# Performance work log

Measured on AMD Instinct MI355X. Metric: run time of the kernel, lower is better.

## Reference

```python
import jax, jax.numpy as jnp
import numpy as np
from functools import partial

B, IN, H, OUT, DEPTH = 4096, 1024, 2048, 1024, 8


def setup_inputs() -> dict:
    key = jax.random.key(0)
    ks = jax.random.split(key, 20)
    r = lambda k, shape: jax.random.normal(k, shape, dtype=jnp.float32)
    return {
        "x":  r(ks[0], (B, IN)),
        "W0": r(ks[1], (IN, H)) / np.sqrt(IN),  "b0": r(ks[2], (H,)) * 0.01,
        "W1": r(ks[3], (H, H)) / np.sqrt(H),    "b1": r(ks[4], (H,)) * 0.01,
        "cw1": r(ks[5], (DEPTH, H, H)), "cb1": r(ks[6], (H,)),
        "KW1": r(ks[7], (H, H)) / np.sqrt(H),  "Kb1": r(ks[8], (H,)) * 0.01,
        "W2": r(ks[9], (H, H)) / np.sqrt(H),   "b2": r(ks[10], (H,)) * 0.01,
        "cw2": r(ks[11], (DEPTH, H, H)), "cb2": r(ks[12], (H,)),
        "KW2": r(ks[13], (H, H)) / np.sqrt(H), "Kb2": r(ks[14], (H,)) * 0.01,
        "W3": r(ks[15], (H, OUT)) / np.sqrt(H), "b3": r(ks[16], (OUT,)) * 0.01,
    }


def _cosmic_processing(cw, batch, n_in, n_out):
    # state starts uniform over the n_in-dim 'cosmic' register, one per output j
    s0 = jnp.full((n_out, n_in), 1.0 / np.sqrt(n_in), dtype=cw.dtype)
    angles = cw[:, :, :3]  # (depth, n_out, 3): consciousness/intelligence/wisdom angles

    def step(s, ang):  # s: (n_out, n_in), ang: (n_out, 3)
        # circulant rotation: (M s)[i] = cos*s[i] - sin*s[i+1] + sin*s[i-1]
        for k in range(3):
            c = jnp.cos(ang[:, k])[:, None]
            si = jnp.sin(ang[:, k])[:, None]
            s = c * s - si * jnp.roll(s, -1, axis=1) + si * jnp.roll(s, 1, axis=1)
        return s, None

    s, _ = jax.lax.scan(step, s0, angles)
    prob = jnp.abs(s[:, 0]) ** 2  # (n_out,), sample-independent
    return jnp.broadcast_to(prob[None, :], (batch, n_out))


def _cosmic_layer(x, cw, cb, KW, Kb):
    classical = x @ KW + Kb
    cosmic = _cosmic_processing(cw, x.shape[0], x.shape[1], KW.shape[1])
    return jnp.tanh(classical + cosmic)


def reference(x, W0, b0, W1, b1, cw1, cb1, KW1, Kb1,
              W2, b2, cw2, cb2, KW2, Kb2, W3, b3):
    h = jax.nn.relu(x @ W0 + b0)
    h = jax.nn.relu(h @ W1 + b1)
    h = _cosmic_layer(h, cw1, cb1, KW1, Kb1)
    h = jax.nn.relu(h @ W2 + b2)
    h = _cosmic_layer(h, cw2, cb2, KW2, Kb2)
    return jax.nn.relu(h @ W3 + b3)
```

## Files before the change

### kernel.cpp

```cpp
#include <hip/hip_runtime.h>
#include <math.h>


typedef _Float16 f16;
typedef _Float16 f16x8 __attribute__((ext_vector_type(8)));
typedef _Float16 f16x4 __attribute__((ext_vector_type(4)));
typedef float f32x4 __attribute__((ext_vector_type(4)));

#define GLD16(gp, lp) __builtin_amdgcn_global_load_lds( \
    (const __attribute__((address_space(1))) unsigned int*)(gp), \
    (__attribute__((address_space(3))) unsigned int*)(lp), 16, 0, 0)

__global__ void cast_f32_f16(const float* __restrict__ in, f16* __restrict__ out, int n4) {
  int i = blockIdx.x * 256 + threadIdx.x;
  if (i < n4) {
    float4 v = ((const float4*)in)[i];
    f16x4 o = { (f16)v.x, (f16)v.y, (f16)v.z, (f16)v.w };
    ((f16x4*)out)[i] = o;
  }
}

struct TD { const float* src; f16* dst; int K; int N; };
struct TD6 { TD d[6]; };

__global__ void cast_transpose6(TD6 a) {
  TD d = a.d[blockIdx.z];
  int bx = blockIdx.x * 32, by = blockIdx.y * 32;
  if (bx >= d.N || by >= d.K) return;
  __shared__ float tile[32][33];
  int tx = threadIdx.x & 31, ty = threadIdx.x >> 5;
#pragma unroll
  for (int r = ty; r < 32; r += 8)
    tile[r][tx] = d.src[(size_t)(by + r) * d.N + bx + tx];
  __syncthreads();
#pragma unroll
  for (int r = ty; r < 32; r += 8)
    d.dst[(size_t)(bx + r) * d.K + by + tx] = (f16)tile[tx][r];
}

__global__ void cosmic_prob(const float* __restrict__ cw, float* __restrict__ prob, int H) {
  int r = blockIdx.x * 256 + threadIdx.x;
  if (r >= H) return;
  float p = 1.0f;
#pragma unroll
  for (int d = 0; d < 8; ++d) {
    const float* a = cw + ((size_t)d * H + r) * H;
    p *= cosf(a[0]) * cosf(a[1]) * cosf(a[2]);
  }
  prob[r] = p * p / (float)H;
}

template <int EPI>
__global__ __launch_bounds__(512, 2)
void gemm_f16(const f16* __restrict__ A, const f16* __restrict__ BT,
              const float* __restrict__ bias, const float* __restrict__ prob,
              f16* __restrict__ Ch, float* __restrict__ Cf,
              int M, int N, int K, int GX) {
  __shared__ f16 lds[3 * 16384 + 3 * 8192];
  f16* As = lds;
  f16* Bs = lds + 3 * 16384;

  const int t = threadIdx.x;

  const int nwg = gridDim.x;
  const int bid = blockIdx.x;
  const int swz = (bid & 7) * (nwg >> 3) + (bid >> 3);
  const int bx = swz % GX;
  const int by = swz / GX;
  const int m0 = by * 256;
  const int n0 = bx * 128;

  auto stage = [&](int kt, int buf) {
    const int k0 = kt << 6;
#pragma unroll
    for (int q = 0; q < 4; ++q) {
      int Fh = q * 4096 + t * 8;
      int r = Fh >> 6;
      int c = (Fh >> 3) & 7;
      const f16* src = A + (size_t)(m0 + r) * K + k0 + ((c ^ (r & 7)) << 3);
      GLD16(src, As + buf * 16384 + Fh);
    }
#pragma unroll
    for (int q = 0; q < 2; ++q) {
      int Fh = q * 4096 + t * 8;
      int r = Fh >> 6;
      int c = (Fh >> 3) & 7;
      const f16* src = BT + (size_t)(n0 + r) * K + k0 + ((c ^ (r & 7)) << 3);
      GLD16(src, Bs + buf * 8192 + Fh);
    }
  };

  const int wave = t >> 6, lane = t & 63;
  const int wr = wave >> 1, wc = wave & 1;
  const int kg = lane >> 4, rc = lane & 15;

  f32x4 acc[4][4] = {};

  auto compute = [&](int buf) {
    const f16* Ab = As + buf * 16384;
    const f16* Bb = Bs + buf * 8192;
    f16x8 af[2][4], bf[2][4];
#pragma unroll
    for (int s = 0; s < 2; ++s) {
      const int cc = s * 4 + kg;
#pragma unroll
      for (int i = 0; i < 4; ++i) {
        int row = wr * 64 + i * 16 + rc;
        af[s][i] = *(const f16x8*)&Ab[row * 64 + ((cc ^ (row & 7)) << 3)];
      }
#pragma unroll
      for (int n = 0; n < 4; ++n) {
        int row = wc * 64 + n * 16 + rc;
        bf[s][n] = *(const f16x8*)&Bb[row * 64 + ((cc ^ (row & 7)) << 3)];
      }
    }
    __builtin_amdgcn_s_setprio(1);
#pragma unroll
    for (int s = 0; s < 2; ++s)
#pragma unroll
      for (int i = 0; i < 4; ++i)
#pragma unroll
        for (int n = 0; n < 4; ++n)
          acc[i][n] = __builtin_amdgcn_mfma_f32_16x16x32_f16(af[s][i], bf[s][n], acc[i][n], 0, 0, 0);
    __builtin_amdgcn_s_setprio(0);
  };

  const int nt = K >> 6;
  stage(0, 0);
  stage(1, 1);
  int cur = 0;
  for (int kt = 0; kt < nt - 1; ++kt) {
    asm volatile("s_waitcnt vmcnt(6) lgkmcnt(0)" ::: "memory");
    __builtin_amdgcn_s_barrier();
    if (kt + 2 < nt) {
      int sb = cur + 2; if (sb >= 3) sb -= 3;
      stage(kt + 2, sb);
    }
    compute(cur);
    cur = (cur + 1 == 3) ? 0 : cur + 1;
  }
  asm volatile("s_waitcnt vmcnt(0) lgkmcnt(0)" ::: "memory");
  __builtin_amdgcn_s_barrier();
  compute(cur);

#pragma unroll
  for (int n = 0; n < 4; ++n) {
    const int col = n0 + wc * 64 + n * 16 + rc;
    float bn = bias[col];
    if (EPI == 1) bn += prob[col];
#pragma unroll
    for (int i = 0; i < 4; ++i) {
      const int row = m0 + wr * 64 + i * 16 + kg * 4;
#pragma unroll
      for (int q = 0; q < 4; ++q) {
        float v = acc[i][n][q] + bn;
        if (EPI == 1) v = tanhf(v);
        else v = fmaxf(v, 0.0f);
        if (EPI == 2) Cf[(size_t)(row + q) * N + col] = v;
        else Ch[(size_t)(row + q) * N + col] = (f16)v;
      }
    }
  }
}

extern "C" void kernel_launch(void* const* d_in, const int* in_sizes, int n_in,
                              void* d_out, int out_size, void* d_ws, size_t ws_size,
                              hipStream_t stream) {
  const float* x   = (const float*)d_in[0];
  const float* W0  = (const float*)d_in[1];
  const float* b0  = (const float*)d_in[2];
  const float* W1  = (const float*)d_in[3];
  const float* b1  = (const float*)d_in[4];
  const float* cw1 = (const float*)d_in[5];
  const float* KW1 = (const float*)d_in[7];
  const float* Kb1 = (const float*)d_in[8];
  const float* W2  = (const float*)d_in[9];
  const float* b2  = (const float*)d_in[10];
  const float* cw2 = (const float*)d_in[11];
  const float* KW2 = (const float*)d_in[13];
  const float* Kb2 = (const float*)d_in[14];
  const float* W3  = (const float*)d_in[15];
  const float* b3  = (const float*)d_in[16];

  const int B = 4096, IN = 1024, H = 2048, OUT = 1024;

  char* ws = (char*)d_ws;
  size_t off = 0;
  auto alloc = [&](size_t bytes) {
    char* p = ws + off;
    off = (off + bytes + 255) & ~(size_t)255;
    return p;
  };
  f16* xh    = (f16*)alloc((size_t)B * IN * 2);
  f16* W0T   = (f16*)alloc((size_t)H * IN * 2);
  f16* W1T   = (f16*)alloc((size_t)H * H * 2);
  f16* KW1T  = (f16*)alloc((size_t)H * H * 2);
  f16* W2T   = (f16*)alloc((size_t)H * H * 2);
  f16* KW2T  = (f16*)alloc((size_t)H * H * 2);
  f16* W3T   = (f16*)alloc((size_t)OUT * H * 2);
  f16* hA    = (f16*)alloc((size_t)B * H * 2);
  f16* hB    = (f16*)alloc((size_t)B * H * 2);
  float* p1  = (float*)alloc((size_t)H * 4);
  float* p2  = (float*)alloc((size_t)H * 4);
  (void)ws_size;

  cast_f32_f16<<<(B * IN / 4 + 255) / 256, 256, 0, stream>>>(x, xh, B * IN / 4);

  TD6 td;
  td.d[0] = { W0,  W0T,  IN, H };
  td.d[1] = { W1,  W1T,  H,  H };
  td.d[2] = { KW1, KW1T, H,  H };
  td.d[3] = { W2,  W2T,  H,  H };
  td.d[4] = { KW2, KW2T, H,  H };
  td.d[5] = { W3,  W3T,  H,  OUT };
  cast_transpose6<<<dim3(H / 32, H / 32, 6), 256, 0, stream>>>(td);

  cosmic_prob<<<(H + 255) / 256, 256, 0, stream>>>(cw1, p1, H);
  cosmic_prob<<<(H + 255) / 256, 256, 0, stream>>>(cw2, p2, H);

  auto launch = [&](int epi, const f16* Aq, const f16* BTq, const float* bi,
                    const float* pr, f16* Co, float* Cfo, int N_, int K_) {
    int gx = N_ / 128, gy = B / 256;
    dim3 grid(gx * gy);
    if (epi == 0) gemm_f16<0><<<grid, 512, 0, stream>>>(Aq, BTq, bi, pr, Co, Cfo, B, N_, K_, gx);
    else if (epi == 1) gemm_f16<1><<<grid, 512, 0, stream>>>(Aq, BTq, bi, pr, Co, Cfo, B, N_, K_, gx);
    else gemm_f16<2><<<grid, 512, 0, stream>>>(Aq, BTq, bi, pr, Co, Cfo, B, N_, K_, gx);
  };

  launch(0, xh, W0T, b0,  nullptr, hA, nullptr, H,   IN);
  launch(0, hA, W1T, b1,  nullptr, hB, nullptr, H,   H);
  launch(1, hB, KW1T, Kb1, p1,     hA, nullptr, H,   H);
  launch(0, hA, W2T, b2,  nullptr, hB, nullptr, H,   H);
  launch(1, hB, KW2T, Kb2, p2,     hA, nullptr, H,   H);
  launch(2, hA, W3T, b3,  nullptr, nullptr, (float*)d_out, OUT, H);
}
```

Baseline: 249.9 us.

## Switch GEMM to 32x32x16 MFMA with interleaved staging and smaller final tile

```diff
diff --git a/kernel.cpp b/kernel.cpp
--- a/kernel.cpp
+++ b/kernel.cpp
@@ -5,7 +5,7 @@
 typedef _Float16 f16;
 typedef _Float16 f16x8 __attribute__((ext_vector_type(8)));
 typedef _Float16 f16x4 __attribute__((ext_vector_type(4)));
-typedef float f32x4 __attribute__((ext_vector_type(4)));
+typedef float f32x16 __attribute__((ext_vector_type(16)));
 
 #define GLD16(gp, lp) __builtin_amdgcn_global_load_lds( \
     (const __attribute__((address_space(1))) unsigned int*)(gp), \
@@ -38,27 +38,34 @@
     d.dst[(size_t)(bx + r) * d.K + by + tx] = (f16)tile[tx][r];
 }
 
-__global__ void cosmic_prob(const float* __restrict__ cw, float* __restrict__ prob, int H) {
+__global__ void cosmic_pp(const float* __restrict__ cw, float* __restrict__ pp, int H) {
+  int i = blockIdx.x * 256 + threadIdx.x;
+  if (i >= 8 * H) return;
+  const float* a = cw + (size_t)i * H;
+  pp[i] = cosf(a[0]) * cosf(a[1]) * cosf(a[2]);
+}
+__global__ void cosmic_fin(const float* __restrict__ pp, float* __restrict__ prob, int H) {
   int r = blockIdx.x * 256 + threadIdx.x;
   if (r >= H) return;
   float p = 1.0f;
 #pragma unroll
-  for (int d = 0; d < 8; ++d) {
-    const float* a = cw + ((size_t)d * H + r) * H;
-    p *= cosf(a[0]) * cosf(a[1]) * cosf(a[2]);
-  }
+  for (int d = 0; d < 8; ++d) p *= pp[d * H + r];
   prob[r] = p * p / (float)H;
 }
 
-template <int EPI>
+template <int EPI, int BM>
 __global__ __launch_bounds__(512, 2)
 void gemm_f16(const f16* __restrict__ A, const f16* __restrict__ BT,
               const float* __restrict__ bias, const float* __restrict__ prob,
               f16* __restrict__ Ch, float* __restrict__ Cf,
               int M, int N, int K, int GX) {
-  __shared__ f16 lds[3 * 16384 + 3 * 8192];
+  constexpr int ASZ = BM * 64;
+  constexpr int BSZ = 128 * 64;
+  constexpr int MB  = BM / 128;
+  constexpr int RA  = BM / 64;
+  __shared__ f16 lds[3 * (ASZ + BSZ)];
   f16* As = lds;
-  f16* Bs = lds + 3 * 16384;
+  f16* Bs = lds + 3 * ASZ;
 
   const int t = threadIdx.x;
 
@@ -67,97 +74,105 @@
   const int swz = (bid & 7) * (nwg >> 3) + (bid >> 3);
   const int bx = swz % GX;
   const int by = swz / GX;
-  const int m0 = by * 256;
+  const int m0 = by * BM;
   const int n0 = bx * 128;
 
-  auto stage = [&](int kt, int buf) {
-    const int k0 = kt << 6;
-#pragma unroll
-    for (int q = 0; q < 4; ++q) {
-      int Fh = q * 4096 + t * 8;
-      int r = Fh >> 6;
-      int c = (Fh >> 3) & 7;
-      const f16* src = A + (size_t)(m0 + r) * K + k0 + ((c ^ (r & 7)) << 3);
-      GLD16(src, As + buf * 16384 + Fh);
-    }
-#pragma unroll
-    for (int q = 0; q < 2; ++q) {
-      int Fh = q * 4096 + t * 8;
-      int r = Fh >> 6;
-      int c = (Fh >> 3) & 7;
-      const f16* src = BT + (size_t)(n0 + r) * K + k0 + ((c ^ (r & 7)) << 3);
-      GLD16(src, Bs + buf * 8192 + Fh);
-    }
+  auto stageA = [&](int kt, int buf, int q) {
+    int F = q * 4096 + t * 8;
+    int r = F >> 6, c = (F >> 3) & 7;
+    const f16* src = A + (size_t)(m0 + r) * K + (kt << 6) + ((c ^ (r & 7)) << 3);
+    GLD16(src, As + buf * ASZ + F);
+  };
+  auto stageB = [&](int kt, int buf, int q) {
+    int F = q * 4096 + t * 8;
+    int r = F >> 6, c = (F >> 3) & 7;
+    const f16* src = BT + (size_t)(n0 + r) * K + (kt << 6) + ((c ^ (r & 7)) << 3);
+    GLD16(src, Bs + buf * BSZ + F);
+  };
+  auto stage_all = [&](int kt, int buf) {
+#pragma unroll
+    for (int q = 0; q < RA; ++q) stageA(kt, buf, q);
+#pragma unroll
+    for (int q = 0; q < 2; ++q) stageB(kt, buf, q);
   };
 
   const int wave = t >> 6, lane = t & 63;
   const int wr = wave >> 1, wc = wave & 1;
-  const int kg = lane >> 4, rc = lane & 15;
-
-  f32x4 acc[4][4] = {};
-
-  auto compute = [&](int buf) {
-    const f16* Ab = As + buf * 16384;
-    const f16* Bb = Bs + buf * 8192;
-    f16x8 af[2][4], bf[2][4];
-#pragma unroll
-    for (int s = 0; s < 2; ++s) {
-      const int cc = s * 4 + kg;
-#pragma unroll
-      for (int i = 0; i < 4; ++i) {
-        int row = wr * 64 + i * 16 + rc;
-        af[s][i] = *(const f16x8*)&Ab[row * 64 + ((cc ^ (row & 7)) << 3)];
+  const int rc = lane & 31, hi = lane >> 5;
+
+  f32x16 acc[MB][2] = {};
+
+  auto kphase = [&](int cur, int p, int stage_kt, int sb) {
+    const f16* Ab = As + cur * ASZ;
+    const f16* Bb = Bs + cur * BSZ;
+    const int cc = p * 2 + hi;
+    f16x8 a[MB], b[2];
+#pragma unroll
+    for (int mb = 0; mb < MB; ++mb) {
+      int row = wr * (BM / 4) + mb * 32 + rc;
+      a[mb] = *(const f16x8*)&Ab[row * 64 + ((cc ^ (row & 7)) << 3)];
+    }
+#pragma unroll
+    for (int nb = 0; nb < 2; ++nb) {
+      int row = wc * 64 + nb * 32 + rc;
+      b[nb] = *(const f16x8*)&Bb[row * 64 + ((cc ^ (row & 7)) << 3)];
+    }
+    if (stage_kt >= 0) {
+      if (BM == 256) {
+        stageA(stage_kt, sb, p);
+        if (p < 2) stageB(stage_kt, sb, p);
+      } else {
+        if (p < 2) stageA(stage_kt, sb, p);
+        else stageB(stage_kt, sb, p - 2);
       }
-#pragma unroll
-      for (int n = 0; n < 4; ++n) {
-        int row = wc * 64 + n * 16 + rc;
-        bf[s][n] = *(const f16x8*)&Bb[row * 64 + ((cc ^ (row & 7)) << 3)];
-      }
-    }
+    }
+    asm volatile("s_waitcnt lgkmcnt(0)" ::: "memory");
+    __builtin_amdgcn_sched_barrier(0);
     __builtin_amdgcn_s_setprio(1);
 #pragma unroll
-    for (int s = 0; s < 2; ++s)
-#pragma unroll
-      for (int i = 0; i < 4; ++i)
-#pragma unroll
-        for (int n = 0; n < 4; ++n)
-          acc[i][n] = __builtin_amdgcn_mfma_f32_16x16x32_f16(af[s][i], bf[s][n], acc[i][n], 0, 0, 0);
+    for (int mb = 0; mb < MB; ++mb)
+#pragma unroll
+      for (int nb = 0; nb < 2; ++nb)
+        acc[mb][nb] = __builtin_amdgcn_mfma_f32_32x32x16_f16(a[mb], b[nb], acc[mb][nb], 0, 0, 0);
     __builtin_amdgcn_s_setprio(0);
+    __builtin_amdgcn_sched_barrier(0);
   };
 
   const int nt = K >> 6;
-  stage(0, 0);
-  stage(1, 1);
+  stage_all(0, 0);
+  stage_all(1, 1);
   int cur = 0;
-  for (int kt = 0; kt < nt - 1; ++kt) {
-    asm volatile("s_waitcnt vmcnt(6) lgkmcnt(0)" ::: "memory");
+  for (int kt = 0; kt < nt; ++kt) {
+    if (kt + 1 < nt) {
+      if (BM == 256) asm volatile("s_waitcnt vmcnt(6)" ::: "memory");
+      else           asm volatile("s_waitcnt vmcnt(4)" ::: "memory");
+    } else {
+      asm volatile("s_waitcnt vmcnt(0)" ::: "memory");
+    }
     __builtin_amdgcn_s_barrier();
-    if (kt + 2 < nt) {
-      int sb = cur + 2; if (sb >= 3) sb -= 3;
-      stage(kt + 2, sb);
-    }
-    compute(cur);
+    int sb = cur + 2; if (sb >= 3) sb -= 3;
+    const int skt = (kt + 2 < nt) ? (kt + 2) : -1;
+#pragma unroll
+    for (int p = 0; p < 4; ++p) kphase(cur, p, skt, sb);
     cur = (cur + 1 == 3) ? 0 : cur + 1;
   }
-  asm volatile("s_waitcnt vmcnt(0) lgkmcnt(0)" ::: "memory");
-  __builtin_amdgcn_s_barrier();
-  compute(cur);
-
-#pragma unroll
-  for (int n = 0; n < 4; ++n) {
-    const int col = n0 + wc * 64 + n * 16 + rc;
+
+#pragma unroll
+  for (int nb = 0; nb < 2; ++nb) {
+    const int col = n0 + wc * 64 + nb * 32 + rc;
     float bn = bias[col];
     if (EPI == 1) bn += prob[col];
 #pragma unroll
-    for (int i = 0; i < 4; ++i) {
-      const int row = m0 + wr * 64 + i * 16 + kg * 4;
-#pragma unroll
-      for (int q = 0; q < 4; ++q) {
-        float v = acc[i][n][q] + bn;
+    for (int mb = 0; mb < MB; ++mb) {
+      const int rbase = m0 + wr * (BM / 4) + mb * 32 + 4 * hi;
+#pragma unroll
+      for (int r = 0; r < 16; ++r) {
+        const int row = rbase + (r & 3) + 8 * (r >> 2);
+        float v = acc[mb][nb][r] + bn;
         if (EPI == 1) v = tanhf(v);
         else v = fmaxf(v, 0.0f);
-        if (EPI == 2) Cf[(size_t)(row + q) * N + col] = v;
-        else Ch[(size_t)(row + q) * N + col] = (f16)v;
+        if (EPI == 2) Cf[(size_t)row * N + col] = v;
+        else Ch[(size_t)row * N + col] = (f16)v;
       }
     }
   }
@@ -202,6 +217,7 @@
   f16* hB    = (f16*)alloc((size_t)B * H * 2);
   float* p1  = (float*)alloc((size_t)H * 4);
   float* p2  = (float*)alloc((size_t)H * 4);
+  float* pp  = (float*)alloc((size_t)8 * H * 4);
   (void)ws_size;
 
   cast_f32_f16<<<(B * IN / 4 + 255) / 256, 256, 0, stream>>>(x, xh, B * IN / 4);
@@ -215,22 +231,23 @@
   td.d[5] = { W3,  W3T,  H,  OUT };
   cast_transpose6<<<dim3(H / 32, H / 32, 6), 256, 0, stream>>>(td);
 
-  cosmic_prob<<<(H + 255) / 256, 256, 0, stream>>>(cw1, p1, H);
-  cosmic_prob<<<(H + 255) / 256, 256, 0, stream>>>(cw2, p2, H);
-
-  auto launch = [&](int epi, const f16* Aq, const f16* BTq, const float* bi,
-                    const float* pr, f16* Co, float* Cfo, int N_, int K_) {
-    int gx = N_ / 128, gy = B / 256;
-    dim3 grid(gx * gy);
-    if (epi == 0) gemm_f16<0><<<grid, 512, 0, stream>>>(Aq, BTq, bi, pr, Co, Cfo, B, N_, K_, gx);
-    else if (epi == 1) gemm_f16<1><<<grid, 512, 0, stream>>>(Aq, BTq, bi, pr, Co, Cfo, B, N_, K_, gx);
-    else gemm_f16<2><<<grid, 512, 0, stream>>>(Aq, BTq, bi, pr, Co, Cfo, B, N_, K_, gx);
-  };
-
-  launch(0, xh, W0T, b0,  nullptr, hA, nullptr, H,   IN);
-  launch(0, hA, W1T, b1,  nullptr, hB, nullptr, H,   H);
-  launch(1, hB, KW1T, Kb1, p1,     hA, nullptr, H,   H);
-  launch(0, hA, W2T, b2,  nullptr, hB, nullptr, H,   H);
-  launch(1, hB, KW2T, Kb2, p2,     hA, nullptr, H,   H);
-  launch(2, hA, W3T, b3,  nullptr, nullptr, (float*)d_out, OUT, H);
-}
+  cosmic_pp<<<(8 * H + 255) / 256, 256, 0, stream>>>(cw1, pp, H);
+  cosmic_fin<<<(H + 255) / 256, 256, 0, stream>>>(pp, p1, H);
+  cosmic_pp<<<(8 * H + 255) / 256, 256, 0, stream>>>(cw2, pp, H);
+  cosmic_fin<<<(H + 255) / 256, 256, 0, stream>>>(pp, p2, H);
+
+  {
+    int gx = H / 128, gy = B / 256;
+    dim3 g(gx * gy);
+    gemm_f16<0, 256><<<g, 512, 0, stream>>>(xh, W0T, b0,  nullptr, hA, nullptr, B, H, IN, gx);
+    gemm_f16<0, 256><<<g, 512, 0, stream>>>(hA, W1T, b1,  nullptr, hB, nullptr, B, H, H,  gx);
+    gemm_f16<1, 256><<<g, 512, 0, stream>>>(hB, KW1T, Kb1, p1,     hA, nullptr, B, H, H,  gx);
+    gemm_f16<0, 256><<<g, 512, 0, stream>>>(hA, W2T, b2,  nullptr, hB, nullptr, B, H, H,  gx);
+    gemm_f16<1, 256><<<g, 512, 0, stream>>>(hB, KW2T, Kb2, p2,     hA, nullptr, B, H, H,  gx);
+  }
+  {
+    int gx = OUT / 128, gy = B / 128;
+    dim3 g(gx * gy);
+    gemm_f16<2, 128><<<g, 512, 0, stream>>>(hA, W3T, b3, nullptr, nullptr, (float*)d_out, B, OUT, H, gx);
+  }
+}
```

Result: faster. 234.2 us (-6.3%).
